# Kernel tuning notes

Hardware: AMD Instinct MI355X
Metric: run time of the kernel (lower is better)

## Reference

```python
import jax, jax.numpy as jnp
import numpy as np


def setup_inputs() -> dict:
    key = jax.random.key(0)
    ks = jax.random.split(key, 7)
    S, N, D_in, D_out = 8, 5000, 128, 128
    theta = jax.random.uniform(ks[0], (S,), dtype=jnp.float32)
    T_slices = jax.random.normal(ks[1], (S, N, N), dtype=jnp.float32)
    x = jax.random.normal(ks[2], (N, D_in), dtype=jnp.float32)
    a = (jax.random.uniform(ks[3], (N, N), dtype=jnp.float32) < 0.05).astype(jnp.float32)
    # PReLU per-feature slope (torch default init is 0.25; random here)
    alpha = jax.random.uniform(ks[4], (D_in,), dtype=jnp.float32) * 0.5
    W = jax.random.normal(ks[5], (D_out, D_in), dtype=jnp.float32) * (1.0 / np.sqrt(D_in))
    b = jax.random.normal(ks[6], (D_out,), dtype=jnp.float32) * 0.01
    return {"theta": theta, "T_slices": T_slices, "x": x, "a": a,
            "alpha": alpha, "W": W, "b": b}


def reference(theta, T_slices, x, a, alpha, W, b):
    # weighted sum of diffusion slices: q[i,j] = sum_s theta[s] * T[s,i,j]
    q = jnp.einsum('s,sij->ij', theta, T_slices)
    q = q * a  # elementwise mask (sparsification pattern)
    out = q @ x  # dense matmul == sparse.mm on masked matrix (same math)
    # PReLU with per-feature (last-dim) slopes
    out = jnp.where(out >= 0, out, alpha * out)
    # Linear: out @ W.T + b
    return out @ W.T + b
```

## Files before the change

### kernel.cpp

```cpp
#include <hip/hip_runtime.h>

#define SS 8
#define NN 5000
#define NNSQ 25000000
#define DD 128
#define RB 8
#define JS 4
#define JT 128
#define TPB 10
#define QS 132
#define RG 625

typedef float f4 __attribute__((ext_vector_type(4)));

typedef const __attribute__((address_space(1))) void glb_void;
typedef __attribute__((address_space(3))) void lds_void;

__device__ __forceinline__ void gld_lds16(const void* g, void* l) {
    __builtin_amdgcn_global_load_lds((glb_void*)g, (lds_void*)l, 16, 0, 0);
}

__global__ __launch_bounds__(256, 2)
void diffuse_spmm(const float* __restrict__ theta,
                  const float* __restrict__ Tm,
                  const float* __restrict__ x,
                  const float* __restrict__ am,
                  float* __restrict__ ws)
{
    __shared__ float stage[9 * RB * 128];
    __shared__ float qv[2][RB * QS];
    __shared__ float red[3 * RB * 128];

    const int t    = threadIdx.x;
    const int wid  = t >> 6;
    const int lane = t & 63;
    const int rg   = blockIdx.x % RG;
    const int js   = blockIdx.x / RG;
    const int i0   = rg * RB;
    const int tile0 = js * TPB;

    const int ar = (wid << 1) + (lane >> 5);
    const int aj = (lane & 31) << 2;
    const int slot = t & 31;
    const int h    = t >> 5;
    const int d0   = slot << 2;

    float th[SS];
#pragma unroll
    for (int s = 0; s < SS; ++s) th[s] = theta[s];

    auto stage_dma = [&](int tt) {
        const int j = tt * JT + aj;
        if (j < NN) {
            const size_t goff = (size_t)(i0 + ar) * NN + j;
#pragma unroll
            for (int s = 0; s < SS; ++s)
                gld_lds16(Tm + (size_t)s * NNSQ + goff,
                          &stage[s * (RB * 128) + (wid << 1) * 128]);
            gld_lds16(am + goff, &stage[SS * (RB * 128) + (wid << 1) * 128]);
        }
    };

    auto qcompute = [&](int tt, int n) {
        const int j = tt * JT + aj;
        const int lbase = ar * 128 + aj;
        f4 ssum = (*(const f4*)&stage[0 * (RB * 128) + lbase]) * th[0];
#pragma unroll
        for (int s = 1; s < SS; ++s)
            ssum += (*(const f4*)&stage[s * (RB * 128) + lbase]) * th[s];
        f4 av = *(const f4*)&stage[SS * (RB * 128) + lbase];
        f4 q  = av * ssum;
        if (j >= NN) q = (f4)(0.0f);
        *(f4*)&qv[n][ar * QS + aj] = q;
    };

    f4 acc[RB];
#pragma unroll
    for (int r = 0; r < RB; ++r) acc[r] = (f4)(0.0f);

    stage_dma(tile0);
    asm volatile("s_waitcnt vmcnt(0)" ::: "memory");
    __builtin_amdgcn_sched_barrier(0);
    qcompute(tile0, 0);
    __syncthreads();

    for (int k = 0; k < TPB; ++k) {
        const int tt = tile0 + k;

        f4 xv[16];
        {
            const int jb = tt * JT + (h << 4);
#pragma unroll
            for (int q = 0; q < 16; ++q) {
                const int j = jb + q;
                if (j < NN) xv[q] = *(const f4*)(x + (size_t)j * DD + d0);
                else        xv[q] = (f4)(0.0f);
            }
        }
        __builtin_amdgcn_sched_barrier(0);
        if (k + 1 < TPB) stage_dma(tt + 1);
        __builtin_amdgcn_sched_barrier(0);

        const float* qp = &qv[k & 1][0];
#pragma unroll
        for (int qc = 0; qc < 4; ++qc) {
#pragma unroll
            for (int r = 0; r < RB; ++r) {
                f4 q = *(const f4*)&qp[r * QS + (h << 4) + (qc << 2)];
                acc[r] += q.x * xv[qc * 4 + 0];
                acc[r] += q.y * xv[qc * 4 + 1];
                acc[r] += q.z * xv[qc * 4 + 2];
                acc[r] += q.w * xv[qc * 4 + 3];
            }
        }

        if (k + 1 < TPB) {
            asm volatile("s_waitcnt vmcnt(0)" ::: "memory");
            __builtin_amdgcn_sched_barrier(0);
            qcompute(tt + 1, (k + 1) & 1);
            __syncthreads();
        }
    }

#pragma unroll
    for (int r = 0; r < RB; ++r)
#pragma unroll
        for (int c = 0; c < 4; ++c)
            acc[r][c] += __shfl_xor(acc[r][c], 32);

    const int w = t >> 6;
    if (w > 0 && (t & 63) < 32) {
#pragma unroll
        for (int r = 0; r < RB; ++r)
            *(f4*)&red[((w - 1) * RB + r) * 128 + d0] = acc[r];
    }
    __syncthreads();
    if (w == 0 && (t & 63) < 32) {
#pragma unroll
        for (int r = 0; r < RB; ++r) {
            f4 v = acc[r];
#pragma unroll
            for (int p = 0; p < 3; ++p)
                v += *(const f4*)&red[(p * RB + r) * 128 + d0];
            *(f4*)&ws[(((size_t)js * RG + rg) * RB + r) * DD + d0] = v;
        }
    }
}

__global__ __launch_bounds__(256, 2)
void prelu_linear(const float* __restrict__ alpha,
                  const float* __restrict__ W,
                  const float* __restrict__ b,
                  const float* __restrict__ ws,
                  float* __restrict__ out)
{
    __shared__ float Wt[128 * 129];
    __shared__ float p[16 * 128];
    const int t  = threadIdx.x;
    const int i0 = blockIdx.x * 16;

#pragma unroll
    for (int it = 0; it < 16; ++it) {
        int f  = (it * 256 + t) * 4;
        int d  = f >> 7;
        int kk = f & 127;
        f4 w4 = *(const f4*)(W + f);
        Wt[(kk + 0) * 129 + d] = w4.x;
        Wt[(kk + 1) * 129 + d] = w4.y;
        Wt[(kk + 2) * 129 + d] = w4.z;
        Wt[(kk + 3) * 129 + d] = w4.w;
    }

#pragma unroll
    for (int it = 0; it < 2; ++it) {
        int fi  = it * 256 + t;
        int row = i0 + (fi >> 5);
        int dc  = (fi & 31) << 2;
        if (row < NN) {
            size_t base = (size_t)row * DD + dc;
            f4 v = *(const f4*)(ws + base);
            v += *(const f4*)(ws + base + (size_t)1 * RG * RB * DD);
            v += *(const f4*)(ws + base + (size_t)2 * RG * RB * DD);
            v += *(const f4*)(ws + base + (size_t)3 * RG * RB * DD);
            f4 al = *(const f4*)(alpha + dc);
            f4 pv;
            pv.x = v.x >= 0.f ? v.x : al.x * v.x;
            pv.y = v.y >= 0.f ? v.y : al.y * v.y;
            pv.z = v.z >= 0.f ? v.z : al.z * v.z;
            pv.w = v.w >= 0.f ? v.w : al.w * v.w;
            *(f4*)&p[(row - i0) * 128 + dc] = pv;
        }
    }
    __syncthreads();

    const int d  = t & 127;
    const int rq = t >> 7;
    const float bv = b[d];
    float acc[8];
#pragma unroll
    for (int ri = 0; ri < 8; ++ri) acc[ri] = 0.f;
#pragma unroll 8
    for (int k = 0; k < 128; ++k) {
        float wv = Wt[k * 129 + d];
#pragma unroll
        for (int ri = 0; ri < 8; ++ri)
            acc[ri] += p[(rq * 8 + ri) * 128 + k] * wv;
    }
#pragma unroll
    for (int ri = 0; ri < 8; ++ri) {
        int row = i0 + rq * 8 + ri;
        if (row < NN) out[(size_t)row * DD + d] = acc[ri] + bv;
    }
}

extern "C" void kernel_launch(void* const* d_in, const int* in_sizes, int n_in,
                              void* d_out, int out_size, void* d_ws, size_t ws_size,
                              hipStream_t stream) {
    const float* theta = (const float*)d_in[0];
    const float* T     = (const float*)d_in[1];
    const float* x     = (const float*)d_in[2];
    const float* a     = (const float*)d_in[3];
    const float* alpha = (const float*)d_in[4];
    const float* W     = (const float*)d_in[5];
    const float* b     = (const float*)d_in[6];
    float* out = (float*)d_out;
    float* ws  = (float*)d_ws;

    dim3 blk(256);
    dim3 g1(RG * JS);
    diffuse_spmm<<<g1, blk, 0, stream>>>(theta, T, x, a, ws);

    dim3 g2((NN + 15) / 16);
    prelu_linear<<<g2, blk, 0, stream>>>(alpha, W, b, ws, out);
}
```

Measured before the change: 232.4 us.

## Double-buffer T slice staging two tiles ahead and load mask via registers

After: 276.6 us. +19.0%, slower.

```diff
diff --git a/kernel.cpp b/kernel.cpp
--- a/kernel.cpp
+++ b/kernel.cpp
@@ -8,7 +8,6 @@
 #define JS 4
 #define JT 128
 #define TPB 10
-#define QS 132
 #define RG 625
 
 typedef float f4 __attribute__((ext_vector_type(4)));
@@ -19,6 +18,11 @@
 __device__ __forceinline__ void gld_lds16(const void* g, void* l) {
     __builtin_amdgcn_global_load_lds((glb_void*)g, (lds_void*)l, 16, 0, 0);
 }
+
+#define VMCNT9  asm volatile("s_waitcnt vmcnt(9)" ::: "memory")
+#define VMCNT0  asm volatile("s_waitcnt vmcnt(0)" ::: "memory")
+#define LGKM0   asm volatile("s_waitcnt lgkmcnt(0)" ::: "memory")
+#define SB0     __builtin_amdgcn_sched_barrier(0)
 
 __global__ __launch_bounds__(256, 2)
 void diffuse_spmm(const float* __restrict__ theta,
@@ -27,9 +31,8 @@
                   const float* __restrict__ am,
                   float* __restrict__ ws)
 {
-    __shared__ float stage[9 * RB * 128];
-    __shared__ float qv[2][RB * QS];
-    __shared__ float red[3 * RB * 128];
+    __shared__ float stg[2][SS * RB * 128];
+    __shared__ float qv[2][RB * 128];
 
     const int t    = threadIdx.x;
     const int wid  = t >> 6;
@@ -41,55 +44,62 @@
 
     const int ar = (wid << 1) + (lane >> 5);
     const int aj = (lane & 31) << 2;
-    const int slot = t & 31;
-    const int h    = t >> 5;
-    const int d0   = slot << 2;
+    const int h  = t >> 5;
+    const int d0 = (t & 31) << 2;
 
     float th[SS];
 #pragma unroll
     for (int s = 0; s < SS; ++s) th[s] = theta[s];
 
-    auto stage_dma = [&](int tt) {
-        const int j = tt * JT + aj;
+    auto stage_dma = [&](int m) {
+        const int j = (tile0 + m) * JT + aj;
         if (j < NN) {
             const size_t goff = (size_t)(i0 + ar) * NN + j;
 #pragma unroll
             for (int s = 0; s < SS; ++s)
                 gld_lds16(Tm + (size_t)s * NNSQ + goff,
-                          &stage[s * (RB * 128) + (wid << 1) * 128]);
-            gld_lds16(am + goff, &stage[SS * (RB * 128) + (wid << 1) * 128]);
+                          &stg[m & 1][s * (RB * 128) + (wid << 1) * 128]);
         }
     };
 
-    auto qcompute = [&](int tt, int n) {
-        const int j = tt * JT + aj;
+    auto aload = [&](int m) -> f4 {
+        const int j = (tile0 + m) * JT + aj;
+        f4 v = (f4)(0.0f);
+        if (j < NN) v = *(const f4*)(am + (size_t)(i0 + ar) * NN + j);
+        return v;
+    };
+
+    auto qcompute = [&](int m, f4 sa) {
+        const int j = (tile0 + m) * JT + aj;
         const int lbase = ar * 128 + aj;
-        f4 ssum = (*(const f4*)&stage[0 * (RB * 128) + lbase]) * th[0];
+        f4 ssum = (*(const f4*)&stg[m & 1][0 * (RB * 128) + lbase]) * th[0];
 #pragma unroll
         for (int s = 1; s < SS; ++s)
-            ssum += (*(const f4*)&stage[s * (RB * 128) + lbase]) * th[s];
-        f4 av = *(const f4*)&stage[SS * (RB * 128) + lbase];
-        f4 q  = av * ssum;
+            ssum += (*(const f4*)&stg[m & 1][s * (RB * 128) + lbase]) * th[s];
+        f4 q = sa * ssum;
         if (j >= NN) q = (f4)(0.0f);
-        *(f4*)&qv[n][ar * QS + aj] = q;
+        *(f4*)&qv[m & 1][ar * 128 + aj] = q;
     };
 
     f4 acc[RB];
 #pragma unroll
     for (int r = 0; r < RB; ++r) acc[r] = (f4)(0.0f);
 
-    stage_dma(tile0);
-    asm volatile("s_waitcnt vmcnt(0)" ::: "memory");
-    __builtin_amdgcn_sched_barrier(0);
-    qcompute(tile0, 0);
-    __syncthreads();
+    stage_dma(0);
+    f4 a0 = aload(0);
+    SB0;
+    stage_dma(1);
+    SB0;
+    VMCNT9;
+    SB0;
+    qcompute(0, a0);
+    LGKM0;
+    __builtin_amdgcn_s_barrier();
 
     for (int k = 0; k < TPB; ++k) {
-        const int tt = tile0 + k;
-
         f4 xv[16];
         {
-            const int jb = tt * JT + (h << 4);
+            const int jb = (tile0 + k) * JT + (h << 4);
 #pragma unroll
             for (int q = 0; q < 16; ++q) {
                 const int j = jb + q;
@@ -97,16 +107,18 @@
                 else        xv[q] = (f4)(0.0f);
             }
         }
-        __builtin_amdgcn_sched_barrier(0);
-        if (k + 1 < TPB) stage_dma(tt + 1);
-        __builtin_amdgcn_sched_barrier(0);
+        f4 sa = (f4)(0.0f);
+        if (k + 1 < TPB) sa = aload(k + 1);
+        SB0;
+        if (k + 2 < TPB) stage_dma(k + 2);
+        SB0;
 
         const float* qp = &qv[k & 1][0];
 #pragma unroll
         for (int qc = 0; qc < 4; ++qc) {
 #pragma unroll
             for (int r = 0; r < RB; ++r) {
-                f4 q = *(const f4*)&qp[r * QS + (h << 4) + (qc << 2)];
+                f4 q = *(const f4*)&qp[r * 128 + (h << 4) + (qc << 2)];
                 acc[r] += q.x * xv[qc * 4 + 0];
                 acc[r] += q.y * xv[qc * 4 + 1];
                 acc[r] += q.z * xv[qc * 4 + 2];
@@ -115,10 +127,11 @@
         }
 
         if (k + 1 < TPB) {
-            asm volatile("s_waitcnt vmcnt(0)" ::: "memory");
-            __builtin_amdgcn_sched_barrier(0);
-            qcompute(tt + 1, (k + 1) & 1);
-            __syncthreads();
+            if (k + 2 < TPB) { VMCNT9; } else { VMCNT0; }
+            SB0;
+            qcompute(k + 1, sa);
+            LGKM0;
+            __builtin_amdgcn_s_barrier();
         }
     }
 
@@ -128,14 +141,15 @@
         for (int c = 0; c < 4; ++c)
             acc[r][c] += __shfl_xor(acc[r][c], 32);
 
-    const int w = t >> 6;
-    if (w > 0 && (t & 63) < 32) {
+    float* red = &stg[0][0];
+    __syncthreads();
+    if (wid > 0 && lane < 32) {
 #pragma unroll
         for (int r = 0; r < RB; ++r)
-            *(f4*)&red[((w - 1) * RB + r) * 128 + d0] = acc[r];
+            *(f4*)&red[((wid - 1) * RB + r) * 128 + d0] = acc[r];
     }
     __syncthreads();
-    if (w == 0 && (t & 63) < 32) {
+    if (wid == 0 && lane < 32) {
 #pragma unroll
         for (int r = 0; r < RB; ++r) {
             f4 v = acc[r];
```
